# Kernel optimization log

Measured on AMD Instinct MI355X. Metric: run time of the kernel, lower is better.

Reference implementation:

```python
import jax, jax.numpy as jnp
import numpy as np

B, T, I = 4, 4096, 1024
HEADS, DIM = 16, 64


def _combine(a, b):
    # Log-sum-exp stable combine of running softmax-attention triples.
    # a, b: tuples (m, u, w) with m,u: (B,T,H), w: (B,T,H,D)
    ma, ua, wa = a
    mb, ub, wb = b
    m = jnp.maximum(ma, mb)
    ea = jnp.exp(ma - m)
    eb = jnp.exp(mb - m)
    u = ua * ea + ub * eb
    w = wa * ea[..., None] + wb * eb[..., None]
    return (m, u, w)


def setup_inputs() -> dict:
    key = jax.random.key(0)
    k1, k2, k3 = jax.random.split(key, 3)
    inputs = jax.random.normal(k1, (B, T, I), dtype=jnp.float32)
    # glorot-ish scale for kernels
    kv_kernel = jax.random.normal(k2, (I, HEADS, DIM, 2), dtype=jnp.float32) * (1.0 / np.sqrt(I))
    q_kernel = jax.random.normal(k3, (HEADS, DIM), dtype=jnp.float32) * (1.0 / np.sqrt(DIM))
    return {"inputs": inputs, "kv_kernel": kv_kernel, "q_kernel": q_kernel, "training": 0}


def reference(inputs, kv_kernel, q_kernel, training):
    # kv projection: (B,T,I) x (I,H,D,2) -> (B,T,H,D,2)
    kv = jnp.einsum('bti,ihdk->bthdk', inputs, kv_kernel)
    kv = jax.nn.silu(kv)  # activation='silu'; dropout is identity at inference
    k = kv[..., 0]  # (B,T,H,D)
    v = kv[..., 1]  # (B,T,H,D)
    # per-head learned query: scores (B,T,H)
    s = jnp.einsum('hd,bthd->bth', q_kernel, k)
    # initial triples per timestep: (m=s, u=1, w=v)
    m0 = s
    u0 = jnp.ones_like(s)
    w0 = v
    m, u, w = jax.lax.associative_scan(_combine, (m0, u0, w0), axis=1)
    # prefix softmax attention output: numerator / denominator -> (B,T,H,D)
    return w / u[..., None]
```

## Files before the change

kernel.cpp:

```cpp
#include <hip/hip_runtime.h>
#include <hip/hip_bf16.h>
#include <stdint.h>

#define B_ 4
#define T_ 4096
#define I_ 1024
#define H_ 16
#define D_ 64
#define M_TOT (B_*T_)
#define N_TOT (H_*D_*2)
#define K_TOT I_

#define BM 256
#define BN 256
#define BK 32
#define NT (K_TOT/BK)
#define BUFE (BM*BK + BN*BK)

typedef __bf16 bf16;
typedef __attribute__((ext_vector_type(8))) __bf16 bf16x8;
typedef __attribute__((ext_vector_type(4))) float f32x4;

#define AS_G __attribute__((address_space(1)))
#define AS_L __attribute__((address_space(3)))

__device__ __forceinline__ void gld_lds16(const void* g, void* l) {
    __builtin_amdgcn_global_load_lds((const AS_G void*)g, (AS_L void*)l, 16, 0, 0);
}

__global__ void k_prep(const float* __restrict__ x, const float* __restrict__ w,
                       bf16* __restrict__ xb, bf16* __restrict__ wt) {
    if (blockIdx.x < 2048) {
        int idx = blockIdx.x * 256 + threadIdx.x;
        const int n4 = (M_TOT * K_TOT) / 4;
        for (int i = idx; i < n4; i += 2048 * 256) {
            float4 f = reinterpret_cast<const float4*>(x)[i];
            union { bf16 h[4]; uint64_t u; } pk;
            pk.h[0] = (bf16)f.x; pk.h[1] = (bf16)f.y; pk.h[2] = (bf16)f.z; pk.h[3] = (bf16)f.w;
            reinterpret_cast<uint64_t*>(xb)[i] = pk.u;
        }
    } else {
        __shared__ float tile[32][33];
        int bid = blockIdx.x - 2048;
        int tn = bid % (N_TOT/32);
        int ti = bid / (N_TOT/32);
        int tid = threadIdx.x;
        int c = tid & 31, rgrp = tid >> 5;
        #pragma unroll
        for (int p = 0; p < 4; ++p) {
            int il = p * 8 + rgrp;
            int cn = tn*32 + c;
            int h = cn >> 7, k2 = (cn >> 6) & 1, d = cn & 63;
            int nsrc = (h << 7) + (d << 1) + k2;
            tile[il][c] = w[(ti*32 + il) * N_TOT + nsrc];
        }
        __syncthreads();
        #pragma unroll
        for (int p = 0; p < 4; ++p) {
            int nl = p * 8 + rgrp;
            wt[(size_t)(tn*32 + nl) * K_TOT + ti*32 + c] = (bf16)tile[c][nl];
        }
    }
}

__device__ __forceinline__ bf16x8 frag(const bf16* base, int row, int g) {
    const char* p = (const char*)base + row * 64 + (((g ^ ((row >> 1) & 3)) & 3) << 4);
    return *reinterpret_cast<const bf16x8*>(p);
}

__global__ __launch_bounds__(512, 2)
void k_gemm(const bf16* __restrict__ xb, const bf16* __restrict__ wt,
            const float* __restrict__ q, bf16* __restrict__ v,
            float* __restrict__ s, float* __restrict__ agg) {
    extern __shared__ __attribute__((aligned(16))) char smem[];
    bf16* lds = (bf16*)smem;
    float* s_lds = (float*)(smem + 4*BUFE*2);

    const int tid = threadIdx.x;
    const int wid = tid >> 6, lane = tid & 63;
    const int wm = wid >> 2, wn = wid & 3;
    const int g = lane >> 4, r16 = lane & 15;

    int bid = blockIdx.x;
    int swz = (bid & 7) * 64 + (bid >> 3);
    int bm = swz >> 3, bn = swz & 7;
    const int row0 = bm * BM, n0 = bn * BN;

    auto stageA = [&](int t) {
        bf16* dst = lds + (t & 3) * BUFE;
        int k0 = t * BK;
        #pragma unroll
        for (int j = 0; j < 2; ++j) {
            int c = j * 512 + tid;
            int row = c >> 2, sl = c & 3;
            int koff = ((sl ^ ((row >> 1) & 3)) & 3) << 3;
            gld_lds16(xb + (size_t)(row0 + row) * K_TOT + k0 + koff, (char*)dst + c * 16);
        }
    };
    auto stageB = [&](int t) {
        bf16* dst = lds + (t & 3) * BUFE + BM * BK;
        int k0 = t * BK;
        #pragma unroll
        for (int j = 0; j < 2; ++j) {
            int c = j * 512 + tid;
            int row = c >> 2, sl = c & 3;
            int koff = ((sl ^ ((row >> 1) & 3)) & 3) << 3;
            gld_lds16(wt + (size_t)(n0 + row) * K_TOT + k0 + koff, (char*)dst + c * 16);
        }
    };

    f32x4 acc[8][4];
    #pragma unroll
    for (int i = 0; i < 8; ++i)
        #pragma unroll
        for (int j = 0; j < 4; ++j) acc[i][j] = (f32x4){0.f,0.f,0.f,0.f};

    stageA(0); stageB(0);
    stageA(1); stageB(1);
    stageA(2); stageB(2);
    asm volatile("s_waitcnt vmcnt(8)" ::: "memory");
    __builtin_amdgcn_s_barrier();

    #pragma unroll 1
    for (int t = 0; t < NT; ++t) {
        const bf16* Ab = lds + (t & 3) * BUFE;
        const bf16* Bb = Ab + BM * BK;
        const bool st = (t + 3 < NT);
        bf16x8 a[4], b[4];

        #pragma unroll
        for (int mi = 0; mi < 4; ++mi) a[mi] = frag(Ab, wm*128 + mi*16 + r16, g);
        #pragma unroll
        for (int ni = 0; ni < 4; ++ni) b[ni] = frag(Bb, wn*64 + ni*16 + r16, g);
        if (st) stageA(t + 3);
        __builtin_amdgcn_s_barrier();
        __builtin_amdgcn_s_setprio(1);
        #pragma unroll
        for (int mi = 0; mi < 4; ++mi)
            #pragma unroll
            for (int ni = 0; ni < 4; ++ni)
                acc[mi][ni] = __builtin_amdgcn_mfma_f32_16x16x32_bf16(a[mi], b[ni], acc[mi][ni], 0,0,0);
        __builtin_amdgcn_s_setprio(0);
        __builtin_amdgcn_s_barrier();

        #pragma unroll
        for (int mi = 0; mi < 4; ++mi) a[mi] = frag(Ab, wm*128 + (mi+4)*16 + r16, g);
        if (st) stageB(t + 3);
        __builtin_amdgcn_s_barrier();
        __builtin_amdgcn_s_setprio(1);
        #pragma unroll
        for (int mi = 0; mi < 4; ++mi)
            #pragma unroll
            for (int ni = 0; ni < 4; ++ni)
                acc[mi+4][ni] = __builtin_amdgcn_mfma_f32_16x16x32_bf16(a[mi], b[ni], acc[mi+4][ni], 0,0,0);
        __builtin_amdgcn_s_setprio(0);
        if (t < NT - 1) {
            if (t < NT - 3)       asm volatile("s_waitcnt vmcnt(8)" ::: "memory");
            else if (t == NT - 3) asm volatile("s_waitcnt vmcnt(4)" ::: "memory");
            else                  asm volatile("s_waitcnt vmcnt(0)" ::: "memory");
            __builtin_amdgcn_s_barrier();
        }
    }

    #pragma unroll
    for (int mi = 0; mi < 8; ++mi)
        #pragma unroll
        for (int ni = 0; ni < 4; ++ni)
            #pragma unroll
            for (int r = 0; r < 4; ++r) {
                float x = acc[mi][ni][r];
                acc[mi][ni][r] = x / (1.0f + __expf(-x));
            }

    const int hloc = wn >> 1;
    const int h = bn * 2 + hloc;

    if ((wn & 1) == 0) {
        float qv[4];
        #pragma unroll
        for (int ni = 0; ni < 4; ++ni) qv[ni] = q[h * D_ + ni*16 + r16];
        #pragma unroll
        for (int mi = 0; mi < 8; ++mi) {
            #pragma unroll
            for (int r = 0; r < 4; ++r) {
                float part = acc[mi][0][r]*qv[0] + acc[mi][1][r]*qv[1]
                           + acc[mi][2][r]*qv[2] + acc[mi][3][r]*qv[3];
                part += __shfl_xor(part, 1);
                part += __shfl_xor(part, 2);
                part += __shfl_xor(part, 4);
                part += __shfl_xor(part, 8);
                if (r16 == 0) {
                    int rl = wm*128 + mi*16 + g*4 + r;
                    s[(row0 + rl) * H_ + h] = part;
                    s_lds[hloc*256 + rl] = part;
                }
            }
        }
    } else {
        #pragma unroll
        for (int mi = 0; mi < 8; ++mi)
            #pragma unroll
            for (int ni = 0; ni < 4; ++ni)
                #pragma unroll
                for (int r = 0; r < 4; ++r) {
                    int row = row0 + wm*128 + mi*16 + g*4 + r;
                    v[(size_t)row * (H_*D_) + h*D_ + ni*16 + r16] = (bf16)acc[mi][ni][r];
                }
    }
    __syncthreads();

    if (wn & 1) {
        #pragma unroll
        for (int c = 0; c < 2; ++c) {
            float sv[16];
            #pragma unroll
            for (int mm = 0; mm < 4; ++mm)
                #pragma unroll
                for (int r = 0; r < 4; ++r)
                    sv[mm*4+r] = s_lds[hloc*256 + wm*128 + (c*4+mm)*16 + g*4 + r];
            float m_l = sv[0];
            #pragma unroll
            for (int i = 1; i < 16; ++i) m_l = fmaxf(m_l, sv[i]);
            float u_l = 0.f, w_l[4] = {0.f, 0.f, 0.f, 0.f};
            #pragma unroll
            for (int mm = 0; mm < 4; ++mm)
                #pragma unroll
                for (int r = 0; r < 4; ++r) {
                    float e = __expf(sv[mm*4+r] - m_l);
                    u_l += e;
                    #pragma unroll
                    for (int ni = 0; ni < 4; ++ni)
                        w_l[ni] += e * acc[c*4+mm][ni][r];
                }
            #pragma unroll
            for (int off = 16; off <= 32; off <<= 1) {
                float m2 = __shfl_xor(m_l, off);
                float u2 = __shfl_xor(u_l, off);
                float w2[4];
                #pragma unroll
                for (int ni = 0; ni < 4; ++ni) w2[ni] = __shfl_xor(w_l[ni], off);
                float mn = fmaxf(m_l, m2);
                float ea = __expf(m_l - mn), eb = __expf(m2 - mn);
                u_l = u_l * ea + u2 * eb;
                #pragma unroll
                for (int ni = 0; ni < 4; ++ni) w_l[ni] = w_l[ni]*ea + w2[ni]*eb;
                m_l = mn;
            }
            if (g == 0) {
                int rbase = row0 + wm*128 + c*64;
                int bb = rbase >> 12, tloc = rbase & (T_-1);
                float* a = agg + (size_t)(((bb*H_ + h) << 6) + (tloc >> 6)) * 66;
                if (r16 == 0) { a[0] = m_l; a[1] = u_l; }
                #pragma unroll
                for (int ni = 0; ni < 4; ++ni) a[2 + ni*16 + r16] = w_l[ni];
            }
        }
    }
}

__global__ void k_scanB(const float* __restrict__ agg, float* __restrict__ pre) {
    int p = blockIdx.x;
    int lane = threadIdx.x;
    float wreg[64];
    #pragma unroll
    for (int c = 0; c < 64; ++c) wreg[c] = agg[(size_t)(p*64 + c)*66 + 2 + lane];
    float ml = agg[(size_t)(p*64 + lane)*66];
    float ul = agg[(size_t)(p*64 + lane)*66 + 1];
    float m = -INFINITY, u = 0.f, w = 0.f;
    #pragma unroll
    for (int c = 0; c < 64; ++c) {
        float* o = pre + (size_t)(p*64 + c)*66;
        if (lane == 0) { o[0] = m; o[1] = u; }
        o[2 + lane] = w;
        float ma = __shfl(ml, c), ua = __shfl(ul, c), wa = wreg[c];
        float mn = fmaxf(m, ma);
        float ec = __expf(m - mn), ea = __expf(ma - mn);
        u = u * ec + ua * ea;
        w = w * ec + wa * ea;
        m = mn;
    }
}

__global__ void k_scanC(const float* __restrict__ s, const bf16* __restrict__ v,
                        const float* __restrict__ pre, float* __restrict__ out) {
    int C = blockIdx.x * 4 + (threadIdx.x >> 6);
    int lane = threadIdx.x & 63;
    int p = C >> 6, c = C & 63;
    int b = p >> 4, h = p & 15;
    int rbase = b * T_ + c * 64;
    const bf16* vbase = v + h * D_ + lane;
    const float* pr = pre + C * 66;
    float m = pr[0], u = pr[1], w = pr[2 + lane];
    #pragma unroll 4
    for (int i = 0; i < 64; ++i) {
        int r = rbase + i;
        float sv = s[r * H_ + h];
        float vv = (float)vbase[(size_t)r * (H_*D_)];
        float mn = fmaxf(m, sv);
        float ea = __expf(m - mn);
        float eb = __expf(sv - mn);
        u = u * ea + eb;
        w = w * ea + vv * eb;
        m = mn;
        out[(size_t)r * (H_*D_) + h * D_ + lane] = __fdividef(w, u);
    }
}

extern "C" void kernel_launch(void* const* d_in, const int* in_sizes, int n_in,
                              void* d_out, int out_size, void* d_ws, size_t ws_size,
                              hipStream_t stream) {
    (void)in_sizes; (void)n_in; (void)out_size; (void)ws_size;
    const float* x  = (const float*)d_in[0];
    const float* wk = (const float*)d_in[1];
    const float* qk = (const float*)d_in[2];
    float* out = (float*)d_out;
    char* ws = (char*)d_ws;

    bf16*  xb  = (bf16*) (ws);
    bf16*  wt  = (bf16*) (ws + 33554432ull);
    bf16*  v   = (bf16*) (ws + 37748736ull);
    float* s   = (float*)(ws + 71303168ull);
    float* agg = (float*)(ws + 72351744ull);
    float* pre = (float*)(ws + 73433088ull);

    hipLaunchKernelGGL(k_prep,  dim3(4096), dim3(256), 0, stream, x, wk, xb, wt);
    hipLaunchKernelGGL(k_gemm,  dim3((M_TOT/BM)*(N_TOT/BN)), dim3(512), 4*BUFE*2 + 2048, stream,
                       xb, wt, qk, v, s, agg);
    hipLaunchKernelGGL(k_scanB, dim3(B_*H_), dim3(64), 0, stream, agg, pre);
    hipLaunchKernelGGL(k_scanC, dim3(B_*H_*64/4), dim3(256), 0, stream, s, v, pre, out);
}
```

Measured before the change: 232.9 us.

## Fuse chunk-prefix scan into final scan kernel and fence LDS reads before MFMA

Removes the separate single-wave-per-(batch,head) chunk-prefix kernel. Each chunk-level wave in the final scan now recomputes its own exclusive prefix by folding all preceding chunk aggregates. This eliminates a serial, low-parallelism launch and the pre buffer round trip, at the cost of redundant prefix work (up to 63 combines per chunk, read mostly from cache). The GEMM loop also gains an explicit lgkmcnt(0) wait plus a sched_barrier before each MFMA block, pinning the LDS fragment loads ahead of the math.

```diff
diff --git a/kernel.cpp b/kernel.cpp
--- a/kernel.cpp
+++ b/kernel.cpp
@@ -134,6 +134,8 @@
         for (int ni = 0; ni < 4; ++ni) b[ni] = frag(Bb, wn*64 + ni*16 + r16, g);
         if (st) stageA(t + 3);
         __builtin_amdgcn_s_barrier();
+        asm volatile("s_waitcnt lgkmcnt(0)" ::: "memory");
+        __builtin_amdgcn_sched_barrier(0);
         __builtin_amdgcn_s_setprio(1);
         #pragma unroll
         for (int mi = 0; mi < 4; ++mi)
@@ -147,6 +149,8 @@
         for (int mi = 0; mi < 4; ++mi) a[mi] = frag(Ab, wm*128 + (mi+4)*16 + r16, g);
         if (st) stageB(t + 3);
         __builtin_amdgcn_s_barrier();
+        asm volatile("s_waitcnt lgkmcnt(0)" ::: "memory");
+        __builtin_amdgcn_sched_barrier(0);
         __builtin_amdgcn_s_setprio(1);
         #pragma unroll
         for (int mi = 0; mi < 4; ++mi)
@@ -258,39 +262,27 @@
     }
 }
 
-__global__ void k_scanB(const float* __restrict__ agg, float* __restrict__ pre) {
-    int p = blockIdx.x;
-    int lane = threadIdx.x;
-    float wreg[64];
-    #pragma unroll
-    for (int c = 0; c < 64; ++c) wreg[c] = agg[(size_t)(p*64 + c)*66 + 2 + lane];
-    float ml = agg[(size_t)(p*64 + lane)*66];
-    float ul = agg[(size_t)(p*64 + lane)*66 + 1];
+__global__ void k_scanC(const float* __restrict__ s, const bf16* __restrict__ v,
+                        const float* __restrict__ agg, float* __restrict__ out) {
+    int C = blockIdx.x * 4 + (threadIdx.x >> 6);
+    int lane = threadIdx.x & 63;
+    int p = C >> 6, c = C & 63;
+    int b = p >> 4, h = p & 15;
+    int rbase = b * T_ + c * 64;
+
     float m = -INFINITY, u = 0.f, w = 0.f;
-    #pragma unroll
-    for (int c = 0; c < 64; ++c) {
-        float* o = pre + (size_t)(p*64 + c)*66;
-        if (lane == 0) { o[0] = m; o[1] = u; }
-        o[2 + lane] = w;
-        float ma = __shfl(ml, c), ua = __shfl(ul, c), wa = wreg[c];
+    const float* ag = agg + (size_t)p * 64 * 66;
+    for (int j = 0; j < c; ++j) {
+        const float* a = ag + j * 66;
+        float ma = a[0], ua = a[1], wa = a[2 + lane];
         float mn = fmaxf(m, ma);
         float ec = __expf(m - mn), ea = __expf(ma - mn);
         u = u * ec + ua * ea;
         w = w * ec + wa * ea;
         m = mn;
     }
-}
-
-__global__ void k_scanC(const float* __restrict__ s, const bf16* __restrict__ v,
-                        const float* __restrict__ pre, float* __restrict__ out) {
-    int C = blockIdx.x * 4 + (threadIdx.x >> 6);
-    int lane = threadIdx.x & 63;
-    int p = C >> 6, c = C & 63;
-    int b = p >> 4, h = p & 15;
-    int rbase = b * T_ + c * 64;
+
     const bf16* vbase = v + h * D_ + lane;
-    const float* pr = pre + C * 66;
-    float m = pr[0], u = pr[1], w = pr[2 + lane];
     #pragma unroll 4
     for (int i = 0; i < 64; ++i) {
         int r = rbase + i;
@@ -321,11 +313,9 @@
     bf16*  v   = (bf16*) (ws + 37748736ull);
     float* s   = (float*)(ws + 71303168ull);
     float* agg = (float*)(ws + 72351744ull);
-    float* pre = (float*)(ws + 73433088ull);
 
     hipLaunchKernelGGL(k_prep,  dim3(4096), dim3(256), 0, stream, x, wk, xb, wt);
     hipLaunchKernelGGL(k_gemm,  dim3((M_TOT/BM)*(N_TOT/BN)), dim3(512), 4*BUFE*2 + 2048, stream,
                        xb, wt, qk, v, s, agg);
-    hipLaunchKernelGGL(k_scanB, dim3(B_*H_), dim3(64), 0, stream, agg, pre);
-    hipLaunchKernelGGL(k_scanC, dim3(B_*H_*64/4), dim3(256), 0, stream, s, v, pre, out);
-}
+    hipLaunchKernelGGL(k_scanC, dim3(B_*H_*64/4), dim3(256), 0, stream, s, v, agg, out);
+}
```

After: 248.5 us. 6.7% more time.
